# Kernel tuning notes

Measured on AMD Instinct MI355X. Metric: run time of the kernel, lower is better.

## Reference

```python
import jax, jax.numpy as jnp
import numpy as np

THRESH = 0.7
MIN_KEPT_FRAC = 0.5  # max(0.001, 0.5)
LOG_CLAMP = -100.0   # torch BCELoss clamps log terms at -100


def setup_inputs() -> dict:
    key = jax.random.key(0)
    k1, k2 = jax.random.split(key)
    shape = (32, 1, 1024, 1024)
    pred = jax.random.uniform(k1, shape, dtype=jnp.float32, minval=1e-6, maxval=1.0 - 1e-6)
    target = jnp.round(jax.random.uniform(k2, shape, dtype=jnp.float32))  # binary mask
    return {"pred": pred, "target": target}


def reference(pred, target):
    p = pred.reshape(-1)
    t = target.reshape(-1)
    # elementwise BCE with reduction='none' (torch clamps log at -100)
    log_p = jnp.clip(jnp.log(p), LOG_CLAMP, None)
    log_1mp = jnp.clip(jnp.log1p(-p), LOG_CLAMP, None)
    pixel_losses = -(t * log_p + (1.0 - t) * log_1mp)

    n = p.shape[0]
    min_kept = min(int(MIN_KEPT_FRAC * (n - 1)), n - 1)  # static python int
    p_sorted = jnp.sort(p)
    min_value = p_sorted[min_kept]
    threshold = jnp.maximum(min_value, jnp.float32(THRESH))

    # keeping losses whose pred value is below the threshold; mean over kept
    mask = p < threshold
    cnt = jnp.sum(mask).astype(pixel_losses.dtype)
    return jnp.sum(jnp.where(mask, pixel_losses, 0.0)) / cnt
```

## Files before the change

kernel.cpp:

```cpp
#include <hip/hip_runtime.h>

#define THRESH   0.7f
#define BASEU    0x3F333334u
#define NBINS    2048
#define NSUB     4096
#define NTHREADS 256
#define UNR      8
#define MAXBLK   8192
#define NBLK_FB  1024
#define LOG2CLAMP 144.2695040888963f
#define LN2_HI   0.6931471805599453

typedef __attribute__((ext_vector_type(4))) float f32x4;

struct Blk { float sum_lt; unsigned cnt_lt, cnt_eq, pad; };

struct Ws {
  Blk      blk[MAXBLK];
  double   sum_lt, sum_eq, prefix_sum;
  unsigned cnt_lt, cnt_eq;
  unsigned done;
  unsigned fin0, fin1, fin2, fin3;
  unsigned selBin, rank_r, prefix_cnt;
  unsigned Hcnt[NBINS];
  float    Hsum[NBINS];
  unsigned subCnt[NSUB];
  float    subSum[NSUB];
};

__device__ __forceinline__ float bce_loss(float p, float t) {
  float x = (t > 0.5f) ? p : (1.0f - p);
  return fminf(-__logf(x), 100.0f);
}

__global__ void k_main(
    const f32x4* __restrict__ p4, const f32x4* __restrict__ t4,
    Ws* __restrict__ ws, int n) {
  const int nvec = n >> 2;
  const int i0 = blockIdx.x * (NTHREADS * UNR) + threadIdx.x;

  float s_lt = 0.f;
  unsigned c_lt = 0u, c_eq = 0u;

#define CONS(PV, TV)                                                           \
  _Pragma("unroll") for (int c = 0; c < 4; ++c) {                              \
    float pv = (PV)[c];                                                        \
    float xx = ((TV)[c] > 0.5f) ? pv : (1.0f - pv);                            \
    float l2 = fminf(-__log2f(xx), LOG2CLAMP);                                 \
    bool lt  = (pv < THRESH);                                                  \
    s_lt += lt ? l2 : 0.0f;                                                    \
    c_lt += lt ? 1u : 0u;                                                      \
    c_eq += (pv == THRESH) ? 1u : 0u;                                          \
  }

  if (i0 + (UNR - 1) * NTHREADS < nvec) {
    f32x4 pv0 = p4[i0 + 0 * NTHREADS], pv1 = p4[i0 + 1 * NTHREADS],
          pv2 = p4[i0 + 2 * NTHREADS], pv3 = p4[i0 + 3 * NTHREADS],
          pv4 = p4[i0 + 4 * NTHREADS], pv5 = p4[i0 + 5 * NTHREADS],
          pv6 = p4[i0 + 6 * NTHREADS], pv7 = p4[i0 + 7 * NTHREADS];
    f32x4 tv0 = t4[i0 + 0 * NTHREADS], tv1 = t4[i0 + 1 * NTHREADS],
          tv2 = t4[i0 + 2 * NTHREADS], tv3 = t4[i0 + 3 * NTHREADS],
          tv4 = t4[i0 + 4 * NTHREADS], tv5 = t4[i0 + 5 * NTHREADS],
          tv6 = t4[i0 + 6 * NTHREADS], tv7 = t4[i0 + 7 * NTHREADS];
    asm volatile("" ::
        "v"(pv0), "v"(pv1), "v"(pv2), "v"(pv3),
        "v"(pv4), "v"(pv5), "v"(pv6), "v"(pv7),
        "v"(tv0), "v"(tv1), "v"(tv2), "v"(tv3),
        "v"(tv4), "v"(tv5), "v"(tv6), "v"(tv7));
    CONS(pv0, tv0) CONS(pv1, tv1) CONS(pv2, tv2) CONS(pv3, tv3)
    CONS(pv4, tv4) CONS(pv5, tv5) CONS(pv6, tv6) CONS(pv7, tv7)
  } else {
#pragma unroll
    for (int u = 0; u < UNR; ++u) {
      int id = i0 + u * NTHREADS;
      if (id < nvec) {
        f32x4 p = p4[id];
        f32x4 t = t4[id];
        CONS(p, t)
      }
    }
    int i = (nvec << 2) + threadIdx.x;
    if (blockIdx.x == gridDim.x - 1 && i < n) {
      float pv = ((const float*)p4)[i];
      float tv = ((const float*)t4)[i];
      float xx = (tv > 0.5f) ? pv : (1.0f - pv);
      float l2 = fminf(-__log2f(xx), LOG2CLAMP);
      if (pv < THRESH)       { c_lt++; s_lt += l2; }
      else if (pv == THRESH) { c_eq++; }
    }
  }
#undef CONS

#pragma unroll
  for (int off = 32; off > 0; off >>= 1) {
    s_lt += __shfl_down(s_lt, off);
    c_lt += __shfl_down(c_lt, off);
    c_eq += __shfl_down(c_eq, off);
  }
  __shared__ float    red_slt[4];
  __shared__ unsigned red_clt[4], red_ceq[4];
  int wave = threadIdx.x >> 6;
  if ((threadIdx.x & 63) == 0) {
    red_slt[wave] = s_lt; red_clt[wave] = c_lt; red_ceq[wave] = c_eq;
  }
  __syncthreads();
  if (threadIdx.x == 0) {
    Blk b;
    b.sum_lt = red_slt[0] + red_slt[1] + red_slt[2] + red_slt[3];
    b.cnt_lt = red_clt[0] + red_clt[1] + red_clt[2] + red_clt[3];
    b.cnt_eq = red_ceq[0] + red_ceq[1] + red_ceq[2] + red_ceq[3];
    b.pad = 0u;
    ws->blk[blockIdx.x] = b;
  }
}

__global__ __launch_bounds__(1024) void k_decide(
    float* __restrict__ out, Ws* __restrict__ ws, int nblk, int kidx) {
  double s_lt = 0.0;
  unsigned long long c_lt = 0, c_eq = 0;
  for (int i = threadIdx.x; i < nblk; i += 1024) {
    Blk b = ws->blk[i];
    s_lt += (double)b.sum_lt;
    c_lt += b.cnt_lt; c_eq += b.cnt_eq;
  }
#pragma unroll
  for (int off = 32; off > 0; off >>= 1) {
    s_lt += __shfl_down(s_lt, off);
    c_lt += __shfl_down(c_lt, off);
    c_eq += __shfl_down(c_eq, off);
  }
  __shared__ double rs[16];
  __shared__ unsigned long long rc[16], re[16];
  int wave = threadIdx.x >> 6;
  if ((threadIdx.x & 63) == 0) { rs[wave] = s_lt; rc[wave] = c_lt; re[wave] = c_eq; }
  __syncthreads();
  if (threadIdx.x == 0) {
    double slt = 0.0; unsigned long long clt = 0, ceq = 0;
    for (int w = 0; w < 16; ++w) { slt += rs[w]; clt += rc[w]; ceq += re[w]; }
    slt *= LN2_HI;
    ws->sum_lt = slt; ws->sum_eq = 0.0;
    ws->cnt_lt = (unsigned)clt; ws->cnt_eq = (unsigned)ceq;
    ws->fin0 = 0u; ws->fin1 = 0u; ws->fin2 = 0u; ws->fin3 = 0u;
    if (clt + ceq > (unsigned long long)kidx) {
      out[0] = (float)(slt / (double)clt);
      ws->done = 1u;
    } else {
      ws->done = 0u;
    }
  }
}

__device__ void gsync(unsigned* ctr, unsigned goal) {
  __syncthreads();
  if (threadIdx.x == 0) {
    __threadfence();
    atomicAdd(ctr, 1u);
    while (atomicAdd(ctr, 0u) < goal) __builtin_amdgcn_s_sleep(8);
  }
  __syncthreads();
  __threadfence();
}

__global__ __launch_bounds__(NTHREADS) void k_fallback(
    const float* __restrict__ pred, const float* __restrict__ targ,
    float* __restrict__ out, Ws* __restrict__ ws, int n, int kidx) {
  if (ws->done) return;

  __shared__ union {
    struct { unsigned hc[NBINS]; float hs[NBINS]; } l1;
    struct { unsigned sc[NSUB];  float ss[NSUB];  } l2;
  } sh;
  __shared__ float sh_eq;

  const int gtid = blockIdx.x * NTHREADS + threadIdx.x;
  const int gstride = gridDim.x * NTHREADS;

  for (int i = gtid; i < NBINS; i += gstride) { ws->Hcnt[i] = 0u; ws->Hsum[i] = 0.f; }
  for (int i = gtid; i < NSUB;  i += gstride) { ws->subCnt[i] = 0u; ws->subSum[i] = 0.f; }
  gsync(&ws->fin0, gridDim.x);

  for (int i = threadIdx.x; i < NBINS; i += NTHREADS) { sh.l1.hc[i] = 0u; sh.l1.hs[i] = 0.f; }
  if (threadIdx.x == 0) sh_eq = 0.f;
  __syncthreads();
  for (int i = gtid; i < n; i += gstride) {
    float pv = pred[i];
    if (pv >= THRESH) {
      float l = bce_loss(pv, targ[i]);
      if (pv == THRESH) {
        atomicAdd(&sh_eq, l);
      } else {
        unsigned b = (__float_as_uint(pv) - BASEU) >> 12;
        if (b > NBINS - 1) b = NBINS - 1;
        atomicAdd(&sh.l1.hc[b], 1u);
        atomicAdd(&sh.l1.hs[b], l);
      }
    }
  }
  __syncthreads();
  for (int i = threadIdx.x; i < NBINS; i += NTHREADS) {
    if (sh.l1.hc[i])        atomicAdd(&ws->Hcnt[i], sh.l1.hc[i]);
    if (sh.l1.hs[i] != 0.f) atomicAdd(&ws->Hsum[i], sh.l1.hs[i]);
  }
  if (threadIdx.x == 0 && sh_eq != 0.f) atomicAdd(&ws->sum_eq, (double)sh_eq);
  gsync(&ws->fin1, gridDim.x);

  if (blockIdx.x == 0 && threadIdx.x == 0) {
    unsigned long long cum = (unsigned long long)ws->cnt_lt + ws->cnt_eq;
    double csum = ws->sum_lt + ws->sum_eq;
    for (int b = 0; b < NBINS; ++b) {
      unsigned hcnt = atomicAdd(&ws->Hcnt[b], 0u);
      if (cum + hcnt > (unsigned long long)kidx) {
        atomicExch(&ws->selBin, (unsigned)b);
        atomicExch(&ws->rank_r, (unsigned)((unsigned long long)kidx - cum));
        atomicExch(&ws->prefix_cnt, (unsigned)cum);
        ws->prefix_sum = csum;
        break;
      }
      cum  += hcnt;
      csum += (double)atomicAdd(&ws->Hsum[b], 0.f);
    }
  }
  gsync(&ws->fin2, gridDim.x);

  unsigned base = BASEU + (atomicAdd(&ws->selBin, 0u) << 12);
  for (int i = threadIdx.x; i < NSUB; i += NTHREADS) { sh.l2.sc[i] = 0u; sh.l2.ss[i] = 0.f; }
  __syncthreads();
  for (int i = gtid; i < n; i += gstride) {
    unsigned u = __float_as_uint(pred[i]);
    if (u >= base && u < base + NSUB) {
      atomicAdd(&sh.l2.sc[u - base], 1u);
      atomicAdd(&sh.l2.ss[u - base], bce_loss(pred[i], targ[i]));
    }
  }
  __syncthreads();
  for (int i = threadIdx.x; i < NSUB; i += NTHREADS) {
    if (sh.l2.sc[i])         atomicAdd(&ws->subCnt[i], sh.l2.sc[i]);
    if (sh.l2.ss[i] != 0.f)  atomicAdd(&ws->subSum[i], sh.l2.ss[i]);
  }
  gsync(&ws->fin3, gridDim.x);

  if (blockIdx.x == 0 && threadIdx.x == 0) {
    unsigned r = atomicAdd(&ws->rank_r, 0u);
    unsigned long long cum = 0;
    double csum = 0.0;
    for (int i = 0; i < NSUB; ++i) {
      unsigned c = atomicAdd(&ws->subCnt[i], 0u);
      if (cum + c > (unsigned long long)r) {
        unsigned long long cnt_final = (unsigned long long)atomicAdd(&ws->prefix_cnt, 0u) + cum;
        double sum_final = ws->prefix_sum + csum;
        out[0] = (float)(sum_final / (double)cnt_final);
        break;
      }
      cum  += c;
      csum += (double)atomicAdd(&ws->subSum[i], 0.f);
    }
  }
}

extern "C" void kernel_launch(void* const* d_in, const int* in_sizes, int n_in,
                              void* d_out, int out_size, void* d_ws, size_t ws_size,
                              hipStream_t stream) {
  const float* pred = (const float*)d_in[0];
  const float* targ = (const float*)d_in[1];
  float* out = (float*)d_out;
  Ws* ws = (Ws*)d_ws;
  int n = in_sizes[0];
  long long kll = (long long)(n - 1) / 2;
  if (kll > (long long)(n - 1)) kll = n - 1;
  int kidx = (int)kll;

  int nvec = n >> 2;
  int nblk = (nvec + NTHREADS * UNR - 1) / (NTHREADS * UNR);
  if (nblk > MAXBLK) nblk = MAXBLK;
  if (nblk < 1) nblk = 1;

  k_main    <<<nblk, NTHREADS, 0, stream>>>((const f32x4*)pred, (const f32x4*)targ, ws, n);
  k_decide  <<<1, 1024, 0, stream>>>(out, ws, nblk, kidx);
  k_fallback<<<NBLK_FB, NTHREADS, 0, stream>>>(pred, targ, out, ws, n, kidx);
}
```

Before: 279.7 us.

## Use grid-stride loop with nontemporal loads in main reduction kernel

After: 257.3 us. 8.0% less time.

```diff
diff --git a/kernel.cpp b/kernel.cpp
--- a/kernel.cpp
+++ b/kernel.cpp
@@ -5,7 +5,6 @@
 #define NBINS    2048
 #define NSUB     4096
 #define NTHREADS 256
-#define UNR      8
 #define MAXBLK   8192
 #define NBLK_FB  1024
 #define LOG2CLAMP 144.2695040888963f
@@ -37,7 +36,8 @@
     const f32x4* __restrict__ p4, const f32x4* __restrict__ t4,
     Ws* __restrict__ ws, int n) {
   const int nvec = n >> 2;
-  const int i0 = blockIdx.x * (NTHREADS * UNR) + threadIdx.x;
+  const int tid = blockIdx.x * NTHREADS + threadIdx.x;
+  const int stride = gridDim.x * NTHREADS;
 
   float s_lt = 0.f;
   unsigned c_lt = 0u, c_eq = 0u;
@@ -53,43 +53,32 @@
     c_eq += (pv == THRESH) ? 1u : 0u;                                          \
   }
 
-  if (i0 + (UNR - 1) * NTHREADS < nvec) {
-    f32x4 pv0 = p4[i0 + 0 * NTHREADS], pv1 = p4[i0 + 1 * NTHREADS],
-          pv2 = p4[i0 + 2 * NTHREADS], pv3 = p4[i0 + 3 * NTHREADS],
-          pv4 = p4[i0 + 4 * NTHREADS], pv5 = p4[i0 + 5 * NTHREADS],
-          pv6 = p4[i0 + 6 * NTHREADS], pv7 = p4[i0 + 7 * NTHREADS];
-    f32x4 tv0 = t4[i0 + 0 * NTHREADS], tv1 = t4[i0 + 1 * NTHREADS],
-          tv2 = t4[i0 + 2 * NTHREADS], tv3 = t4[i0 + 3 * NTHREADS],
-          tv4 = t4[i0 + 4 * NTHREADS], tv5 = t4[i0 + 5 * NTHREADS],
-          tv6 = t4[i0 + 6 * NTHREADS], tv7 = t4[i0 + 7 * NTHREADS];
-    asm volatile("" ::
-        "v"(pv0), "v"(pv1), "v"(pv2), "v"(pv3),
-        "v"(pv4), "v"(pv5), "v"(pv6), "v"(pv7),
-        "v"(tv0), "v"(tv1), "v"(tv2), "v"(tv3),
-        "v"(tv4), "v"(tv5), "v"(tv6), "v"(tv7));
-    CONS(pv0, tv0) CONS(pv1, tv1) CONS(pv2, tv2) CONS(pv3, tv3)
-    CONS(pv4, tv4) CONS(pv5, tv5) CONS(pv6, tv6) CONS(pv7, tv7)
-  } else {
-#pragma unroll
-    for (int u = 0; u < UNR; ++u) {
-      int id = i0 + u * NTHREADS;
-      if (id < nvec) {
-        f32x4 p = p4[id];
-        f32x4 t = t4[id];
-        CONS(p, t)
-      }
-    }
-    int i = (nvec << 2) + threadIdx.x;
-    if (blockIdx.x == gridDim.x - 1 && i < n) {
-      float pv = ((const float*)p4)[i];
-      float tv = ((const float*)t4)[i];
+  int i = tid;
+  for (; i + stride < nvec; i += 2 * stride) {
+    f32x4 pa = __builtin_nontemporal_load(p4 + i);
+    f32x4 pb = __builtin_nontemporal_load(p4 + i + stride);
+    f32x4 ta = __builtin_nontemporal_load(t4 + i);
+    f32x4 tb = __builtin_nontemporal_load(t4 + i + stride);
+    CONS(pa, ta)
+    CONS(pb, tb)
+  }
+  for (; i < nvec; i += stride) {
+    f32x4 pa = __builtin_nontemporal_load(p4 + i);
+    f32x4 ta = __builtin_nontemporal_load(t4 + i);
+    CONS(pa, ta)
+  }
+#undef CONS
+  {
+    int j = (nvec << 2) + tid;
+    if (j < n) {
+      float pv = ((const float*)p4)[j];
+      float tv = ((const float*)t4)[j];
       float xx = (tv > 0.5f) ? pv : (1.0f - pv);
       float l2 = fminf(-__log2f(xx), LOG2CLAMP);
       if (pv < THRESH)       { c_lt++; s_lt += l2; }
       else if (pv == THRESH) { c_eq++; }
     }
   }
-#undef CONS
 
 #pragma unroll
   for (int off = 32; off > 0; off >>= 1) {
@@ -270,7 +259,7 @@
   int kidx = (int)kll;
 
   int nvec = n >> 2;
-  int nblk = (nvec + NTHREADS * UNR - 1) / (NTHREADS * UNR);
+  int nblk = (nvec + NTHREADS - 1) / NTHREADS;
   if (nblk > MAXBLK) nblk = MAXBLK;
   if (nblk < 1) nblk = 1;
 
```
